# Optimization experiments

Hardware: AMD Instinct MI355X
Metric: run time of the kernel (lower is better)

The kernel has to match this reference:

```python
import jax, jax.numpy as jnp
import numpy as np

N_NODES = 100000
N_EDGES = 3200000
IN_CH = 54
HID = 32        # hidden_channels (concat of 4 heads x 8)
OUT = 64        # out_channels (mean over 4 heads)
HEADS = 4
N_GRAPHS = 512


def _segment_softmax(logits, seg, num_segments):
    # logits: [E, H], seg: [E] target-node index
    m = jax.ops.segment_max(logits, seg, num_segments=num_segments)
    m = jnp.where(jnp.isfinite(m), m, 0.0)
    e = jnp.exp(logits - m[seg])
    s = jax.ops.segment_sum(e, seg, num_segments=num_segments)
    return e / (s[seg] + 1e-16)


def _gatv2(x, src, dst, Wl, bl, Wr, br, att, bias, concat):
    # GATv2Conv (PyG): x_l=lin_l(x), x_r=lin_r(x);
    # e_ij = att . leaky_relu(x_l[j] + x_r[i]); alpha = softmax over incoming edges of i;
    # out_i = sum_j alpha_ij * x_l[j]
    N = x.shape[0]
    H, C = att.shape
    xl = (x @ Wl + bl).reshape(N, H, C)
    xr = (x @ Wr + br).reshape(N, H, C)
    e = jax.nn.leaky_relu(xl[src] + xr[dst], 0.2)       # [E, H, C]
    logits = jnp.einsum('ehc,hc->eh', e, att)            # [E, H]
    alpha = _segment_softmax(logits, dst, N)             # [E, H]
    out = jax.ops.segment_sum(xl[src] * alpha[:, :, None], dst, num_segments=N)  # [N,H,C]
    out = out.reshape(N, H * C) if concat else out.mean(axis=1)
    return out + bias


def setup_inputs() -> dict:
    key = jax.random.key(0)
    ks = jax.random.split(key, 16)
    x = jax.random.normal(ks[0], (N_NODES, IN_CH), dtype=jnp.float32)
    edge_index = jax.random.randint(ks[1], (2, N_EDGES), 0, N_NODES, dtype=jnp.int64 if jax.config.jax_enable_x64 else jnp.int32)
    batch_index = jnp.sort(jax.random.randint(ks[2], (N_NODES,), 0, N_GRAPHS))
    C1 = HID // HEADS  # 8
    s1 = 1.0 / np.sqrt(IN_CH)
    s2 = 1.0 / np.sqrt(HID)
    inp = {
        'x': x, 'edge_index': edge_index, 'batch_index': batch_index,
        # layer 1: GATv2Conv(54 -> 8, heads=4, concat=True)
        'Wl1': jax.random.normal(ks[3], (IN_CH, HEADS * C1)) * s1,
        'bl1': jnp.zeros((HEADS * C1,), jnp.float32),
        'Wr1': jax.random.normal(ks[4], (IN_CH, HEADS * C1)) * s1,
        'br1': jnp.zeros((HEADS * C1,), jnp.float32),
        'att1': jax.random.normal(ks[5], (HEADS, C1)) * (1.0 / np.sqrt(C1)),
        'b1': jnp.zeros((HEADS * C1,), jnp.float32),
        # layer 2: GATv2Conv(32 -> 64, heads=4, concat=False)
        'Wl2': jax.random.normal(ks[6], (HID, HEADS * OUT)) * s2,
        'bl2': jnp.zeros((HEADS * OUT,), jnp.float32),
        'Wr2': jax.random.normal(ks[7], (HID, HEADS * OUT)) * s2,
        'br2': jnp.zeros((HEADS * OUT,), jnp.float32),
        'att2': jax.random.normal(ks[8], (HEADS, OUT)) * (1.0 / np.sqrt(OUT)),
        'b2': jnp.zeros((OUT,), jnp.float32),
    }
    return inp


def reference(x, edge_index, batch_index, Wl1, bl1, Wr1, br1, att1, b1,
              Wl2, bl2, Wr2, br2, att2, b2):
    N = x.shape[0]
    # GATv2Conv adds self-loops by default
    loop = jnp.arange(N, dtype=edge_index.dtype)
    src = jnp.concatenate([edge_index[0], loop])
    dst = jnp.concatenate([edge_index[1], loop])
    h = _gatv2(x, src, dst, Wl1, bl1, Wr1, br1, att1, b1, concat=True)
    h = jax.nn.relu(h)  # BasicGNN inter-layer activation (default 'relu')
    h = _gatv2(h, src, dst, Wl2, bl2, Wr2, br2, att2, b2, concat=False)
    # Mish activation
    h = h * jnp.tanh(jax.nn.softplus(h))
    # global mean pool
    sums = jax.ops.segment_sum(h, batch_index, num_segments=N_GRAPHS)
    cnt = jax.ops.segment_sum(jnp.ones((N,), h.dtype), batch_index, num_segments=N_GRAPHS)
    return sums / jnp.maximum(cnt, 1.0)[:, None]
```

## Files before the change

kernel.cpp:

```cpp
#include <hip/hip_runtime.h>
#include <hip/hip_fp16.h>
#include <cmath>

#define NN 100000
#define NE 3200000
#define ET (NE + NN)
#define IN_CH 54
#define HID 32
#define OUTC 64
#define NG 512
#define CAP 80

__device__ __forceinline__ float lrelu(float v){ return fmaxf(v, 0.2f*v); }
__device__ __forceinline__ float mishf(float v){
    float sp = (v > 20.f) ? v : log1pf(__expf(v));
    return v * tanhf(sp);
}

__global__ void k_bucket(const int* __restrict__ ei, int* __restrict__ deg,
                         int* __restrict__ col){
    int e = blockIdx.x*blockDim.x + threadIdx.x;
    if (e >= ET) return;
    int src = (e < NE) ? ei[e]      : (e - NE);
    int dst = (e < NE) ? ei[NE + e] : (e - NE);
    int p = atomicAdd(&deg[dst], 1);
    if (p < CAP) col[dst*CAP + p] = src;
}

__global__ void k_gemm1(const float* __restrict__ x,
                        const float* __restrict__ Wl, const float* __restrict__ bl,
                        const float* __restrict__ Wr, const float* __restrict__ br,
                        __half* __restrict__ xl1, __half* __restrict__ xr1){
    int node = (blockIdx.x*blockDim.x + threadIdx.x) >> 6;
    int lane = threadIdx.x & 63;
    if (node >= NN) return;
    int c = lane & 31;
    const float* W = (lane < 32) ? Wl : Wr;
    float acc = (lane < 32) ? bl[c] : br[c];
    const float* xrow = x + (size_t)node * IN_CH;
    #pragma unroll 6
    for (int k = 0; k < IN_CH; ++k)
        acc += xrow[k] * W[k*HID + c];
    __half h = __float2half_rn(acc);
    if (lane < 32) xl1[node*HID + c] = h;
    else           xr1[node*HID + c] = h;
}

__global__ void k_edge1(const __half* __restrict__ xl1, const __half* __restrict__ xr1,
                        const float* __restrict__ att, const float* __restrict__ b1,
                        const int* __restrict__ dcnt, const int* __restrict__ col,
                        float* __restrict__ hout){
    int node = (blockIdx.x*blockDim.x + threadIdx.x) >> 6;
    int lane = threadIdx.x & 63;
    if (node >= NN) return;
    int cl = lane & 15;
    int slot = lane >> 4;
    float2 xr = __half22float2(*(const __half2*)&xr1[node*HID + 2*cl]);
    float2 at = *(const float2*)&att[2*cl];
    float s = 0.f, acc0 = 0.f, acc1 = 0.f;
    int deg = min(dcnt[node], CAP);
    int lo = node*CAP, hi = lo + deg;
    int niter = (deg + 3) >> 2;
    int e0 = lo + slot;

    auto eload = [&](int i)->unsigned{
        int e = e0 + 4*i;
        int ec = min(e, hi-1);
        return *(const unsigned*)&xl1[col[ec]*HID + 2*cl];
    };
    auto eproc = [&](unsigned q, bool valid){
        float2 xlv = __half22float2(__builtin_bit_cast(__half2, q));
        float t0 = xlv.x + xr.x, t1 = xlv.y + xr.y;
        float v0 = lrelu(t0), v1 = lrelu(t1);
        float p = v0*at.x + v1*at.y;
        p += __shfl_xor(p, 1);
        p += __shfl_xor(p, 2);
        float w = valid ? __expf(p) : 0.f;
        s    += w;
        acc0 += w * xlv.x;
        acc1 += w * xlv.y;
    };

    unsigned q0 = eload(0); bool v0 = (e0 < hi);
    unsigned q1 = 0;        bool v1 = false;
    if (niter > 1){ q1 = eload(1); v1 = (e0 + 4 < hi); }
    for (int i = 2; i < niter; ++i){
        unsigned q2 = eload(i); bool v2 = (e0 + 4*i < hi);
        eproc(q0, v0);
        q0 = q1; v0 = v1; q1 = q2; v1 = v2;
    }
    eproc(q0, v0);
    if (niter > 1) eproc(q1, v1);

    acc0 += __shfl_xor(acc0, 16); acc0 += __shfl_xor(acc0, 32);
    acc1 += __shfl_xor(acc1, 16); acc1 += __shfl_xor(acc1, 32);
    s    += __shfl_xor(s,    16); s    += __shfl_xor(s,    32);
    if (slot == 0){
        float inv = 1.f / (s + 1e-16f);
        float2 bb = *(const float2*)&b1[2*cl];
        float2 o;
        o.x = fmaxf(acc0*inv + bb.x, 0.f);
        o.y = fmaxf(acc1*inv + bb.y, 0.f);
        *(float2*)&hout[node*HID + 2*cl] = o;
    }
}

__global__ __launch_bounds__(256) void k_gemm2(const float* __restrict__ h,
                        const float* __restrict__ Wl, const float* __restrict__ bl,
                        __half* __restrict__ xl2){
    __shared__ float WS[HID*256];
    for (int i = threadIdx.x; i < HID*256; i += 256) WS[i] = Wl[i];
    __syncthreads();
    int lane = threadIdx.x & 63, wv = threadIdx.x >> 6;
    float4 b4 = *(const float4*)&bl[4*lane];
    int node0 = blockIdx.x * 32 + wv * 8;
    int nend = min(node0 + 8, NN);
    for (int n = node0; n < nend; ++n){
        const float* hr = h + n*HID;
        float4 a = {0.f,0.f,0.f,0.f};
        #pragma unroll 8
        for (int k = 0; k < HID; ++k){
            float hk = hr[k];
            float4 w = *(const float4*)&WS[k*256 + 4*lane];
            a.x += hk*w.x; a.y += hk*w.y; a.z += hk*w.z; a.w += hk*w.w;
        }
        ushort4 u;
        u.x = __half_as_ushort(__float2half_rn(a.x + b4.x));
        u.y = __half_as_ushort(__float2half_rn(a.y + b4.y));
        u.z = __half_as_ushort(__float2half_rn(a.z + b4.z));
        u.w = __half_as_ushort(__float2half_rn(a.w + b4.w));
        *(ushort4*)&xl2[(size_t)n*256 + 4*lane] = u;
    }
}

__global__ __launch_bounds__(256) void k_edge2(const __half* __restrict__ xl2,
                        const float* __restrict__ h,
                        const float* __restrict__ Wr, const float* __restrict__ br,
                        const float* __restrict__ att, const float* __restrict__ b2,
                        const int* __restrict__ dcnt, const int* __restrict__ col,
                        const int* __restrict__ batch,
                        float* __restrict__ pool, float* __restrict__ cnt){
    int node = (blockIdx.x*blockDim.x + threadIdx.x) >> 6;
    int lane = threadIdx.x & 63;
    if (node >= NN) return;

    int co = 4*lane;
    float4 xr4 = *(const float4*)&br[co];
    {
        const float* hr = h + node*HID;
        #pragma unroll 8
        for (int k = 0; k < HID; ++k){
            float hk = hr[k];
            float4 w = *(const float4*)&Wr[k*256 + co];
            xr4.x += hk*w.x; xr4.y += hk*w.y; xr4.z += hk*w.z; xr4.w += hk*w.w;
        }
    }
    float4 at4 = *(const float4*)&att[co];
    float s = 0.f;
    float4 acc = {0.f,0.f,0.f,0.f};
    int deg = min(dcnt[node], CAP);
    int lo = node*CAP, hi = lo + deg;
    int nb = deg >> 2;

    uint2 A0,A1,A2,A3, B0,B1,B2,B3;

#define GLD(P0,P1,P2,P3, e_) do { \
        int s0_ = col[(e_)];   int s1_ = col[(e_)+1]; \
        int s2_ = col[(e_)+2]; int s3_ = col[(e_)+3]; \
        P0 = *(const uint2*)(xl2 + s0_*256 + co); \
        P1 = *(const uint2*)(xl2 + s1_*256 + co); \
        P2 = *(const uint2*)(xl2 + s2_*256 + co); \
        P3 = *(const uint2*)(xl2 + s3_*256 + co); \
    } while(0)

#define PROC1(q) do { \
        float2 f01 = __half22float2(__builtin_bit_cast(__half2, q.x)); \
        float2 f23 = __half22float2(__builtin_bit_cast(__half2, q.y)); \
        float t0 = f01.x + xr4.x, t1 = f01.y + xr4.y; \
        float t2 = f23.x + xr4.z, t3 = f23.y + xr4.w; \
        float v0 = lrelu(t0), v1 = lrelu(t1), v2 = lrelu(t2), v3 = lrelu(t3); \
        float p = v0*at4.x + v1*at4.y + v2*at4.z + v3*at4.w; \
        p += __shfl_xor(p, 1); p += __shfl_xor(p, 2); \
        p += __shfl_xor(p, 4); p += __shfl_xor(p, 8); \
        float w = __expf(p); \
        s += w; \
        acc.x += w*f01.x; acc.y += w*f01.y; acc.z += w*f23.x; acc.w += w*f23.y; \
    } while(0)

#define PROC4(P0,P1,P2,P3) do { PROC1(P0); PROC1(P1); PROC1(P2); PROC1(P3); } while(0)

    int e = lo;
    if (nb > 0){
        GLD(A0,A1,A2,A3, e);
        int b = 1;
        for (; b + 1 < nb; b += 2){
            e += 4; GLD(B0,B1,B2,B3, e);
            PROC4(A0,A1,A2,A3);
            e += 4; GLD(A0,A1,A2,A3, e);
            PROC4(B0,B1,B2,B3);
        }
        if (b < nb){
            e += 4; GLD(B0,B1,B2,B3, e);
            PROC4(A0,A1,A2,A3);
            PROC4(B0,B1,B2,B3);
        } else {
            PROC4(A0,A1,A2,A3);
        }
        e += 4;
    }
    for (; e < hi; ++e){
        int src = col[e];
        uint2 q = *(const uint2*)(xl2 + src*256 + co);
        PROC1(q);
    }
#undef GLD
#undef PROC1
#undef PROC4

    float inv = 1.f / (s + 1e-16f);
    float4 t; t.x = acc.x*inv; t.y = acc.y*inv; t.z = acc.z*inv; t.w = acc.w*inv;
    t.x += __shfl_xor(t.x, 16); t.y += __shfl_xor(t.y, 16);
    t.z += __shfl_xor(t.z, 16); t.w += __shfl_xor(t.w, 16);
    t.x += __shfl_xor(t.x, 32); t.y += __shfl_xor(t.y, 32);
    t.z += __shfl_xor(t.z, 32); t.w += __shfl_xor(t.w, 32);
    if (lane < 16){
        int g = batch[node];
        float4 bb = *(const float4*)&b2[co];
        float o0 = 0.25f*t.x + bb.x;
        float o1 = 0.25f*t.y + bb.y;
        float o2 = 0.25f*t.z + bb.z;
        float o3 = 0.25f*t.w + bb.w;
        float* pg = pool + g*OUTC + co;
        atomicAdd(pg+0, mishf(o0));
        atomicAdd(pg+1, mishf(o1));
        atomicAdd(pg+2, mishf(o2));
        atomicAdd(pg+3, mishf(o3));
        if (lane == 0) atomicAdd(&cnt[g], 1.0f);
    }
}

__global__ void k_pool(const float* __restrict__ pool, const float* __restrict__ cnt,
                       float* __restrict__ out){
    int i = blockIdx.x*blockDim.x + threadIdx.x;
    if (i >= NG*OUTC) return;
    out[i] = pool[i] / fmaxf(cnt[i >> 6], 1.0f);
}

extern "C" void kernel_launch(void* const* d_in, const int* in_sizes, int n_in,
                              void* d_out, int out_size, void* d_ws, size_t ws_size,
                              hipStream_t stream){
    const float* x    = (const float*)d_in[0];
    const int*   ei   = (const int*)  d_in[1];
    const int*   batch= (const int*)  d_in[2];
    const float* Wl1  = (const float*)d_in[3];
    const float* bl1  = (const float*)d_in[4];
    const float* Wr1  = (const float*)d_in[5];
    const float* br1  = (const float*)d_in[6];
    const float* att1 = (const float*)d_in[7];
    const float* b1   = (const float*)d_in[8];
    const float* Wl2  = (const float*)d_in[9];
    const float* bl2  = (const float*)d_in[10];
    const float* Wr2  = (const float*)d_in[11];
    const float* br2  = (const float*)d_in[12];
    const float* att2 = (const float*)d_in[13];
    const float* b2   = (const float*)d_in[14];
    float* out = (float*)d_out;

    char* ws = (char*)d_ws;
    size_t off = 0;
    auto alloc = [&](size_t bytes)->char*{
        char* p = ws + off; off += (bytes + 255) & ~(size_t)255; return p;
    };
    __half* xl1  = (__half*)alloc((size_t)NN*HID*2);
    __half* xr1  = (__half*)alloc((size_t)NN*HID*2);
    float*  hbuf = (float*) alloc((size_t)NN*HID*4);
    __half* xl2  = (__half*)alloc((size_t)NN*256*2);
    int*    deg  = (int*)   alloc((size_t)NN*4);
    int*    col  = (int*)   alloc((size_t)NN*CAP*4);
    float*  pool = (float*) alloc((size_t)NG*OUTC*4);
    float*  cnt  = (float*) alloc((size_t)NG*4);

    hipMemsetAsync(deg,  0, (size_t)NN*4,      stream);
    hipMemsetAsync(pool, 0, (size_t)NG*OUTC*4, stream);
    hipMemsetAsync(cnt,  0, (size_t)NG*4,      stream);

    k_bucket<<<(ET+255)/256, 256, 0, stream>>>(ei, deg, col);
    k_gemm1 <<<(NN+3)/4, 256, 0, stream>>>(x, Wl1, bl1, Wr1, br1, xl1, xr1);
    k_edge1 <<<(NN+3)/4, 256, 0, stream>>>(xl1, xr1, att1, b1, deg, col, hbuf);
    k_gemm2 <<<(NN+31)/32, 256, 0, stream>>>(hbuf, Wl2, bl2, xl2);
    k_edge2 <<<(NN+3)/4, 256, 0, stream>>>(xl2, hbuf, Wr2, br2, att2, b2, deg, col, batch, pool, cnt);
    k_pool  <<<(NG*OUTC+255)/256, 256, 0, stream>>>(pool, cnt, out);
}
```

Baseline: 1.023 ms.

## Bucket incoming edges by source tile to sort neighbor gathers in edge kernels

Edges are bucketed per destination into 16 source-range tiles, each slot holding 16-bit local offsets. The edge kernels rebuild a neighbor list in LDS ordered by source tile, so gathers from xl1/xl2 run in roughly ascending source order for better cache locality. The column array shrinks to ushort, but the count array grows to 16 ints per node, adding memset and atomic-target traffic. A per-tile cap of 16 replaces the old per-node cap of 80, which changes overflow behaviour, and the compaction step adds per-node LDS work and shuffles.

```diff
diff --git a/kernel.cpp b/kernel.cpp
--- a/kernel.cpp
+++ b/kernel.cpp
@@ -9,7 +9,9 @@
 #define HID 32
 #define OUTC 64
 #define NG 512
-#define CAP 80
+#define NT 16
+#define TSZ 6250
+#define PCAP 16
 
 __device__ __forceinline__ float lrelu(float v){ return fmaxf(v, 0.2f*v); }
 __device__ __forceinline__ float mishf(float v){
@@ -17,14 +19,15 @@
     return v * tanhf(sp);
 }
 
-__global__ void k_bucket(const int* __restrict__ ei, int* __restrict__ deg,
-                         int* __restrict__ col){
+__global__ void k_bucket(const int* __restrict__ ei, int* __restrict__ cnt2,
+                         unsigned short* __restrict__ col2){
     int e = blockIdx.x*blockDim.x + threadIdx.x;
     if (e >= ET) return;
     int src = (e < NE) ? ei[e]      : (e - NE);
     int dst = (e < NE) ? ei[NE + e] : (e - NE);
-    int p = atomicAdd(&deg[dst], 1);
-    if (p < CAP) col[dst*CAP + p] = src;
+    int t = (unsigned)src / TSZ;
+    int p = atomicAdd(&cnt2[dst*NT + t], 1);
+    if (p < PCAP) col2[((size_t)dst*NT + t)*PCAP + p] = (unsigned short)(src - t*TSZ);
 }
 
 __global__ void k_gemm1(const float* __restrict__ x,
@@ -48,25 +51,37 @@
 
 __global__ void k_edge1(const __half* __restrict__ xl1, const __half* __restrict__ xr1,
                         const float* __restrict__ att, const float* __restrict__ b1,
-                        const int* __restrict__ dcnt, const int* __restrict__ col,
+                        const int* __restrict__ cnt2, const unsigned short* __restrict__ col2,
                         float* __restrict__ hout){
     int node = (blockIdx.x*blockDim.x + threadIdx.x) >> 6;
     int lane = threadIdx.x & 63;
+    int wv   = threadIdx.x >> 6;
+    __shared__ int elist[4][NT*PCAP];
     if (node >= NN) return;
+
+    int cbase = node*NT;
+    int mycnt = (lane < NT) ? cnt2[cbase + lane] : 0;
+    mycnt = min(mycnt, PCAP);
+    int deg = 0;
+    #pragma unroll
+    for (int t = 0; t < NT; ++t){
+        int c = __shfl(mycnt, t);
+        const unsigned short* cp = col2 + ((size_t)cbase + t)*PCAP;
+        if (lane < c) elist[wv][deg + lane] = t*TSZ + (int)cp[lane];
+        deg += c;
+    }
+
     int cl = lane & 15;
     int slot = lane >> 4;
     float2 xr = __half22float2(*(const __half2*)&xr1[node*HID + 2*cl]);
     float2 at = *(const float2*)&att[2*cl];
     float s = 0.f, acc0 = 0.f, acc1 = 0.f;
-    int deg = min(dcnt[node], CAP);
-    int lo = node*CAP, hi = lo + deg;
     int niter = (deg + 3) >> 2;
-    int e0 = lo + slot;
 
     auto eload = [&](int i)->unsigned{
-        int e = e0 + 4*i;
-        int ec = min(e, hi-1);
-        return *(const unsigned*)&xl1[col[ec]*HID + 2*cl];
+        int idx = min(slot + 4*i, deg-1);
+        int src = elist[wv][idx];
+        return *(const unsigned*)&xl1[src*HID + 2*cl];
     };
     auto eproc = [&](unsigned q, bool valid){
         float2 xlv = __half22float2(__builtin_bit_cast(__half2, q));
@@ -81,11 +96,11 @@
         acc1 += w * xlv.y;
     };
 
-    unsigned q0 = eload(0); bool v0 = (e0 < hi);
+    unsigned q0 = eload(0); bool v0 = (slot < deg);
     unsigned q1 = 0;        bool v1 = false;
-    if (niter > 1){ q1 = eload(1); v1 = (e0 + 4 < hi); }
+    if (niter > 1){ q1 = eload(1); v1 = (slot + 4 < deg); }
     for (int i = 2; i < niter; ++i){
-        unsigned q2 = eload(i); bool v2 = (e0 + 4*i < hi);
+        unsigned q2 = eload(i); bool v2 = (slot + 4*i < deg);
         eproc(q0, v0);
         q0 = q1; v0 = v1; q1 = q2; v1 = v2;
     }
@@ -137,12 +152,26 @@
                         const float* __restrict__ h,
                         const float* __restrict__ Wr, const float* __restrict__ br,
                         const float* __restrict__ att, const float* __restrict__ b2,
-                        const int* __restrict__ dcnt, const int* __restrict__ col,
+                        const int* __restrict__ cnt2, const unsigned short* __restrict__ col2,
                         const int* __restrict__ batch,
                         float* __restrict__ pool, float* __restrict__ cnt){
     int node = (blockIdx.x*blockDim.x + threadIdx.x) >> 6;
     int lane = threadIdx.x & 63;
+    int wv   = threadIdx.x >> 6;
+    __shared__ int elist[4][NT*PCAP];
     if (node >= NN) return;
+
+    int cbase = node*NT;
+    int mycnt = (lane < NT) ? cnt2[cbase + lane] : 0;
+    mycnt = min(mycnt, PCAP);
+    int deg = 0;
+    #pragma unroll
+    for (int t = 0; t < NT; ++t){
+        int c = __shfl(mycnt, t);
+        const unsigned short* cp = col2 + ((size_t)cbase + t)*PCAP;
+        if (lane < c) elist[wv][deg + lane] = t*TSZ + (int)cp[lane];
+        deg += c;
+    }
 
     int co = 4*lane;
     float4 xr4 = *(const float4*)&br[co];
@@ -158,19 +187,16 @@
     float4 at4 = *(const float4*)&att[co];
     float s = 0.f;
     float4 acc = {0.f,0.f,0.f,0.f};
-    int deg = min(dcnt[node], CAP);
-    int lo = node*CAP, hi = lo + deg;
     int nb = deg >> 2;
 
     uint2 A0,A1,A2,A3, B0,B1,B2,B3;
 
 #define GLD(P0,P1,P2,P3, e_) do { \
-        int s0_ = col[(e_)];   int s1_ = col[(e_)+1]; \
-        int s2_ = col[(e_)+2]; int s3_ = col[(e_)+3]; \
-        P0 = *(const uint2*)(xl2 + s0_*256 + co); \
-        P1 = *(const uint2*)(xl2 + s1_*256 + co); \
-        P2 = *(const uint2*)(xl2 + s2_*256 + co); \
-        P3 = *(const uint2*)(xl2 + s3_*256 + co); \
+        int4 i4_ = *(const int4*)&elist[wv][(e_)]; \
+        P0 = *(const uint2*)(xl2 + (size_t)i4_.x*256 + co); \
+        P1 = *(const uint2*)(xl2 + (size_t)i4_.y*256 + co); \
+        P2 = *(const uint2*)(xl2 + (size_t)i4_.z*256 + co); \
+        P3 = *(const uint2*)(xl2 + (size_t)i4_.w*256 + co); \
     } while(0)
 
 #define PROC1(q) do { \
@@ -189,7 +215,7 @@
 
 #define PROC4(P0,P1,P2,P3) do { PROC1(P0); PROC1(P1); PROC1(P2); PROC1(P3); } while(0)
 
-    int e = lo;
+    int e = 0;
     if (nb > 0){
         GLD(A0,A1,A2,A3, e);
         int b = 1;
@@ -208,9 +234,9 @@
         }
         e += 4;
     }
-    for (; e < hi; ++e){
-        int src = col[e];
-        uint2 q = *(const uint2*)(xl2 + src*256 + co);
+    for (; e < deg; ++e){
+        int src = elist[wv][e];
+        uint2 q = *(const uint2*)(xl2 + (size_t)src*256 + co);
         PROC1(q);
     }
 #undef GLD
@@ -271,23 +297,23 @@
     auto alloc = [&](size_t bytes)->char*{
         char* p = ws + off; off += (bytes + 255) & ~(size_t)255; return p;
     };
-    __half* xl1  = (__half*)alloc((size_t)NN*HID*2);
-    __half* xr1  = (__half*)alloc((size_t)NN*HID*2);
-    float*  hbuf = (float*) alloc((size_t)NN*HID*4);
-    __half* xl2  = (__half*)alloc((size_t)NN*256*2);
-    int*    deg  = (int*)   alloc((size_t)NN*4);
-    int*    col  = (int*)   alloc((size_t)NN*CAP*4);
-    float*  pool = (float*) alloc((size_t)NG*OUTC*4);
-    float*  cnt  = (float*) alloc((size_t)NG*4);
-
-    hipMemsetAsync(deg,  0, (size_t)NN*4,      stream);
+    __half*         xl1  = (__half*)        alloc((size_t)NN*HID*2);
+    __half*         xr1  = (__half*)        alloc((size_t)NN*HID*2);
+    float*          hbuf = (float*)         alloc((size_t)NN*HID*4);
+    __half*         xl2  = (__half*)        alloc((size_t)NN*256*2);
+    int*            cnt2 = (int*)           alloc((size_t)NN*NT*4);
+    unsigned short* col2 = (unsigned short*)alloc((size_t)NN*NT*PCAP*2);
+    float*          pool = (float*)         alloc((size_t)NG*OUTC*4);
+    float*          cnt  = (float*)         alloc((size_t)NG*4);
+
+    hipMemsetAsync(cnt2, 0, (size_t)NN*NT*4,   stream);
     hipMemsetAsync(pool, 0, (size_t)NG*OUTC*4, stream);
     hipMemsetAsync(cnt,  0, (size_t)NG*4,      stream);
 
-    k_bucket<<<(ET+255)/256, 256, 0, stream>>>(ei, deg, col);
+    k_bucket<<<(ET+255)/256, 256, 0, stream>>>(ei, cnt2, col2);
     k_gemm1 <<<(NN+3)/4, 256, 0, stream>>>(x, Wl1, bl1, Wr1, br1, xl1, xr1);
-    k_edge1 <<<(NN+3)/4, 256, 0, stream>>>(xl1, xr1, att1, b1, deg, col, hbuf);
+    k_edge1 <<<(NN+3)/4, 256, 0, stream>>>(xl1, xr1, att1, b1, cnt2, col2, hbuf);
     k_gemm2 <<<(NN+31)/32, 256, 0, stream>>>(hbuf, Wl2, bl2, xl2);
-    k_edge2 <<<(NN+3)/4, 256, 0, stream>>>(xl2, hbuf, Wr2, br2, att2, b2, deg, col, batch, pool, cnt);
+    k_edge2 <<<(NN+3)/4, 256, 0, stream>>>(xl2, hbuf, Wr2, br2, att2, b2, cnt2, col2, batch, pool, cnt);
     k_pool  <<<(NG*OUTC+255)/256, 256, 0, stream>>>(pool, cnt, out);
 }
```

New measurement: 1.045 ms. 1.02x slower.
